# Performance work log

Measured on AMD Instinct MI355X. Metric: run time of the kernel, lower is better.

Reference implementation:

```python
import jax, jax.numpy as jnp
import numpy as np
from jax import lax

DECAY = 0.9
EPS = 1e-12  # F.normalize eps

B, IN_C, H, W_SP = 32, 512, 64, 64
CODE, CLASSES, MEM = 256, 4, 20


def setup_inputs() -> dict:
    key = jax.random.key(0)
    k1, k2, k3, k4, k5 = jax.random.split(key, 5)
    feats = jax.random.normal(k1, (B, IN_C, H, W_SP), dtype=jnp.float32)
    preds = jax.random.uniform(k2, (B, 1, H, W_SP), dtype=jnp.float32)
    labels = jax.random.randint(k3, (B,), 0, CLASSES, dtype=jnp.int64)
    # queue buffer, L2-normalized along code dim as in __init__
    q = jax.random.normal(k4, (CLASSES, MEM, CODE), dtype=jnp.float32)
    queue = q / jnp.maximum(jnp.linalg.norm(q, axis=2, keepdims=True), EPS)
    kw, kb = jax.random.split(k5)
    Wp = jax.random.normal(kw, (CODE, IN_C), dtype=jnp.float32) * (1.0 / np.sqrt(IN_C))
    bp = jax.random.normal(kb, (CODE,), dtype=jnp.float32) * 0.01
    return {"feats": feats, "preds": preds, "labels": labels, "flag": 1,
            "queue": queue, "Wp": Wp, "bp": bp}


def _update_queue(keys, preds, labels, queue):
    # keys: [B, C, H, W] projected feats; preds: [B, 1, H, W]; sequential EMA per sample
    masked = keys * preds                      # broadcast mask
    feat = masked.reshape(keys.shape[0], keys.shape[1], -1).mean(axis=2)  # [B, C]

    def step(q, inp):
        f, l = inp                             # f: [C], l: scalar label
        slot = q[l]                            # [M, C]
        logit = slot @ f                       # [M]  (query @ key)
        upd = logit[:, None] * f[None, :]      # [M, C] (logit @ value.T)
        upd = upd / jnp.maximum(jnp.linalg.norm(upd, axis=1, keepdims=True), EPS)
        q = q.at[l].set(DECAY * slot + (1.0 - DECAY) * upd)
        return q, None

    queue, _ = lax.scan(step, queue, (feat, labels))
    return queue


def reference(feats, preds, labels, flag, queue, Wp, bp):
    # 1x1 conv projection: [B,512,H,W] -> [B,256,H,W]
    x = jnp.einsum('bchw,oc->bohw', feats, Wp) + bp[None, :, None, None]
    if flag == 1:  # 'train' phase: no-grad EMA memory update
        queue = _update_queue(x, preds, labels, queue)
    b, c, h, w = x.shape
    k = x.reshape(b, c, h * w)                 # key = value-key spatial feats [B, C, HW]
    q = queue[labels]                          # per-sample class memory [B, M, C]
    logit = jnp.einsum('bmc,bcn->bmn', q, k)   # [B, M, HW]
    attn = jax.nn.softmax(logit, axis=1)       # softmax over memory slots (dim=0 per sample)
    new_feat = jnp.einsum('bmc,bmn->bcn', q, attn).reshape(b, c, h, w)
    return jnp.concatenate([new_feat, x], axis=1)  # [B, 2C, H, W]
```

## Files before the change

kernel.cpp:

```cpp
#include <hip/hip_runtime.h>

typedef __attribute__((ext_vector_type(4))) float floatx4;
typedef __attribute__((ext_vector_type(8))) short bf16x8;
typedef __attribute__((ext_vector_type(2))) unsigned int uintx2;
typedef __attribute__((ext_vector_type(4))) unsigned int uintx4;

#define HW   4096
#define CIN  512
#define CODE 256
#define MEM  20
#define NCLS 4
#define NB   32

__device__ __forceinline__ unsigned bf16rn(float f) {
    unsigned u = __float_as_uint(f);
    return u + 0x7fffu + ((u >> 16) & 1u);
}

__device__ __forceinline__ int swz(int row, int slot) {
    return slot ^ ((row >> 2) & 3);
}

__global__ __launch_bounds__(256, 2) void gemm_proj_bf16x3(
    const float* __restrict__ feats,
    const float* __restrict__ Wp,
    const float* __restrict__ bp,
    float* __restrict__ out)
{
    __shared__ unsigned short lds[2][4][128][32];

    const int b   = blockIdx.z;
    const int n0  = blockIdx.x * 128;
    const int o0  = blockIdx.y * 128;
    const int tid = threadIdx.x;
    const int lane = tid & 63;
    const int wid  = tid >> 6;
    const int wm = (wid >> 1) * 64;
    const int wn = (wid & 1) * 64;
    const int lr = lane & 15;
    const int lg = lane >> 4;

    const int ar = tid >> 3;
    const int ac = tid & 7;
    const int bn = tid & 127;
    const int bk = (tid >> 7) * 16;

    const float* fb = feats + (size_t)b * CIN * HW + n0 + bn;
    const float* wa = Wp + (size_t)(o0 + ar) * CIN + ac * 4;

    floatx4 acc[4][4];
#pragma unroll
    for (int i = 0; i < 4; ++i)
#pragma unroll
        for (int j = 0; j < 4; ++j)
#pragma unroll
            for (int r = 0; r < 4; ++r) acc[i][j][r] = 0.f;

    floatx4 av[4];
    float   bv[16];

#define G_LOAD(K0)                                                            \
    {                                                                         \
        _Pragma("unroll")                                                     \
        for (int i = 0; i < 4; ++i)                                           \
            av[i] = *(const floatx4*)(wa + (size_t)(32 * i) * CIN + (K0));    \
        _Pragma("unroll")                                                     \
        for (int j = 0; j < 16; ++j)                                          \
            bv[j] = fb[(size_t)((K0) + bk + j) * HW];                         \
    }

#define STAGE(BUF)                                                            \
    {                                                                         \
        _Pragma("unroll")                                                     \
        for (int i = 0; i < 4; ++i) {                                         \
            const int m = ar + 32 * i;                                        \
            unsigned h[4], l[4];                                              \
            _Pragma("unroll")                                                 \
            for (int e = 0; e < 4; ++e) {                                     \
                unsigned r = bf16rn(av[i][e]);                                \
                float hf = __uint_as_float(r & 0xffff0000u);                  \
                h[e] = r;                                                     \
                l[e] = bf16rn(av[i][e] - hf);                                 \
            }                                                                 \
            uintx2 tH, tL;                                                    \
            tH[0] = (h[0] >> 16) | (h[1] & 0xffff0000u);                      \
            tH[1] = (h[2] >> 16) | (h[3] & 0xffff0000u);                      \
            tL[0] = (l[0] >> 16) | (l[1] & 0xffff0000u);                      \
            tL[1] = (l[2] >> 16) | (l[3] & 0xffff0000u);                      \
            const int sA = swz(m, ac >> 1) * 8 + (ac & 1) * 4;                \
            *(uintx2*)&lds[BUF][0][m][sA] = tH;                               \
            *(uintx2*)&lds[BUF][1][m][sA] = tL;                               \
        }                                                                     \
        unsigned ph[8], pl[8];                                                \
        _Pragma("unroll")                                                     \
        for (int p = 0; p < 8; ++p) {                                         \
            unsigned r0 = bf16rn(bv[2 * p]), r1 = bf16rn(bv[2 * p + 1]);      \
            float h0 = __uint_as_float(r0 & 0xffff0000u);                     \
            float h1 = __uint_as_float(r1 & 0xffff0000u);                     \
            unsigned q0 = bf16rn(bv[2 * p] - h0);                             \
            unsigned q1 = bf16rn(bv[2 * p + 1] - h1);                         \
            ph[p] = (r0 >> 16) | (r1 & 0xffff0000u);                          \
            pl[p] = (q0 >> 16) | (q1 & 0xffff0000u);                          \
        }                                                                     \
        const int sb2 = (tid >> 7) * 2;                                       \
        _Pragma("unroll")                                                     \
        for (int u = 0; u < 2; ++u) {                                         \
            const int s = swz(bn, sb2 + u) * 8;                               \
            uintx4 tB, tC;                                                    \
            tB[0] = ph[4 * u];     tB[1] = ph[4 * u + 1];                     \
            tB[2] = ph[4 * u + 2]; tB[3] = ph[4 * u + 3];                     \
            tC[0] = pl[4 * u];     tC[1] = pl[4 * u + 1];                     \
            tC[2] = pl[4 * u + 2]; tC[3] = pl[4 * u + 3];                     \
            *(uintx4*)&lds[BUF][2][bn][s] = tB;                               \
            *(uintx4*)&lds[BUF][3][bn][s] = tC;                               \
        }                                                                     \
    }

#define COMPUTE(BUF)                                                          \
    {                                                                         \
        bf16x8 fah[4], fal[4], fbh[4], fbl[4];                                \
        _Pragma("unroll")                                                     \
        for (int i = 0; i < 4; ++i) {                                         \
            const int rm = wm + i * 16 + lr;                                  \
            const int rn = wn + i * 16 + lr;                                  \
            fah[i] = *(const bf16x8*)&lds[BUF][0][rm][swz(rm, lg) * 8];       \
            fal[i] = *(const bf16x8*)&lds[BUF][1][rm][swz(rm, lg) * 8];       \
            fbh[i] = *(const bf16x8*)&lds[BUF][2][rn][swz(rn, lg) * 8];       \
            fbl[i] = *(const bf16x8*)&lds[BUF][3][rn][swz(rn, lg) * 8];       \
        }                                                                     \
        _Pragma("unroll")                                                     \
        for (int i = 0; i < 4; ++i)                                           \
            _Pragma("unroll")                                                 \
            for (int j = 0; j < 4; ++j) {                                     \
                acc[i][j] = __builtin_amdgcn_mfma_f32_16x16x32_bf16(          \
                    fah[i], fbh[j], acc[i][j], 0, 0, 0);                      \
                acc[i][j] = __builtin_amdgcn_mfma_f32_16x16x32_bf16(          \
                    fah[i], fbl[j], acc[i][j], 0, 0, 0);                      \
                acc[i][j] = __builtin_amdgcn_mfma_f32_16x16x32_bf16(          \
                    fal[i], fbh[j], acc[i][j], 0, 0, 0);                      \
            }                                                                 \
    }

    G_LOAD(0);
    STAGE(0);

#pragma unroll 2
    for (int step = 0; step < 16; ++step) {
        const int cb = step & 1;
        __syncthreads();
        if (step < 15) G_LOAD((step + 1) * 32);
        COMPUTE(cb);
        if (step < 15) STAGE(cb ^ 1);
    }

#undef G_LOAD
#undef STAGE
#undef COMPUTE

#pragma unroll
    for (int i = 0; i < 4; ++i) {
#pragma unroll
        for (int r = 0; r < 4; ++r) {
            const int m = o0 + wm + i * 16 + lg * 4 + r;
            const float bias = bp[m];
            float* orow = out + ((size_t)b * 2 * CODE + CODE + m) * HW
                        + n0 + wn + lr;
#pragma unroll
            for (int j = 0; j < 4; ++j)
                orow[j * 16] = acc[i][j][r] + bias;
        }
    }
}

__global__ __launch_bounds__(256) void featmean_kernel(
    const float* __restrict__ preds,
    const float* __restrict__ out,
    float* __restrict__ featbuf)
{
    const int c0 = blockIdx.x * 16;
    const int b  = blockIdx.y;
    const int tid = threadIdx.x;
    const int w = tid >> 6, lane = tid & 63;

    __shared__ float sp[HW];
    const float* prow = preds + (size_t)b * HW;
#pragma unroll
    for (int j = 0; j < 4; ++j)
        *(floatx4*)&sp[tid * 4 + j * 1024] = *(const floatx4*)(prow + tid * 4 + j * 1024);
    __syncthreads();

    for (int cc = 0; cc < 4; ++cc) {
        const int c = c0 + w * 4 + cc;
        const float* xrow = out + ((size_t)b * 2 * CODE + CODE + c) * HW;
        float s = 0.f;
#pragma unroll 4
        for (int j = 0; j < 16; ++j) {
            floatx4 xv = *(const floatx4*)(xrow + lane * 4 + j * 256);
            floatx4 pv = *(const floatx4*)&sp[lane * 4 + j * 256];
            s += xv[0] * pv[0] + xv[1] * pv[1] + xv[2] * pv[2] + xv[3] * pv[3];
        }
        for (int off = 32; off > 0; off >>= 1) s += __shfl_down(s, off, 64);
        if (lane == 0) featbuf[b * CODE + c] = s * (1.f / HW);
    }
}

__global__ __launch_bounds__(256) void scan_kernel(
    const float* __restrict__ queue_in,
    const float* __restrict__ featbuf,
    const int* __restrict__ labels,
    const int* __restrict__ flag,
    float* __restrict__ qbuf)
{
    const int tid = threadIdx.x;
    for (int i = tid; i < NCLS * MEM * CODE; i += 256)
        qbuf[i] = queue_in[i];
    __syncthreads();
    if (*flag != 1) return;

    __shared__ float sf[CODE];
    __shared__ float sred[256];
    __shared__ float slog[MEM];
    __shared__ float scoef[MEM];
    __shared__ float snorm;

    const int w = tid >> 6, lane = tid & 63;

    for (int b = 0; b < NB; ++b) {
        const int l = labels[b] & 3;
        float f = featbuf[b * CODE + tid];
        sf[tid] = f;
        sred[tid] = f * f;
        __syncthreads();
        for (int st = 128; st > 0; st >>= 1) {
            if (tid < st) sred[tid] += sred[tid + st];
            __syncthreads();
        }
        if (tid == 0) snorm = sqrtf(sred[0]);
        __syncthreads();

        float* qrow = qbuf + (size_t)l * MEM * CODE;
        for (int mm = 0; mm < 5; ++mm) {
            int m = w * 5 + mm;
            float p = 0.f;
#pragma unroll
            for (int j = 0; j < 4; ++j) {
                int c = lane + 64 * j;
                p += qrow[m * CODE + c] * sf[c];
            }
            for (int off = 32; off > 0; off >>= 1) p += __shfl_down(p, off, 64);
            if (lane == 0) slog[m] = p;
        }
        __syncthreads();
        if (tid < MEM) {
            float lg = slog[tid];
            float denom = fmaxf(fabsf(lg) * snorm, 1e-12f);
            scoef[tid] = 0.1f * lg / denom;
        }
        __syncthreads();
        for (int m = 0; m < MEM; ++m) {
            int idx = m * CODE + tid;
            qrow[idx] = 0.9f * qrow[idx] + scoef[m] * sf[tid];
        }
        __syncthreads();
    }
}

__global__ __launch_bounds__(256) void attn_kernel(
    const float* __restrict__ qbuf,
    const int* __restrict__ labels,
    float* __restrict__ out)
{
    const int b = blockIdx.y;
    const int n = blockIdx.x * 256 + threadIdx.x;
    const int l = labels[b] & 3;

    __shared__ float sq[MEM * CODE];
    for (int i = threadIdx.x; i < MEM * CODE; i += 256)
        sq[i] = qbuf[(size_t)l * MEM * CODE + i];
    __syncthreads();

    const float* xb = out + ((size_t)b * 2 * CODE + CODE) * HW;

    float lg[MEM];
#pragma unroll
    for (int m = 0; m < MEM; ++m) lg[m] = 0.f;

    for (int c = 0; c < CODE; ++c) {
        float xv = xb[(size_t)c * HW + n];
#pragma unroll
        for (int m = 0; m < MEM; ++m) lg[m] += sq[m * CODE + c] * xv;
    }

    float mx = lg[0];
#pragma unroll
    for (int m = 1; m < MEM; ++m) mx = fmaxf(mx, lg[m]);
    float s = 0.f;
#pragma unroll
    for (int m = 0; m < MEM; ++m) { lg[m] = __expf(lg[m] - mx); s += lg[m]; }
    const float inv = 1.f / s;

    float* ob = out + (size_t)b * 2 * CODE * HW;
    for (int c = 0; c < CODE; ++c) {
        float acc = 0.f;
#pragma unroll
        for (int m = 0; m < MEM; ++m) acc += sq[m * CODE + c] * lg[m];
        ob[(size_t)c * HW + n] = acc * inv;
    }
}

extern "C" void kernel_launch(void* const* d_in, const int* in_sizes, int n_in,
                              void* d_out, int out_size, void* d_ws, size_t ws_size,
                              hipStream_t stream)
{
    const float* feats  = (const float*)d_in[0];
    const float* preds  = (const float*)d_in[1];
    const int*   labels = (const int*)d_in[2];
    const int*   flag   = (const int*)d_in[3];
    const float* queue  = (const float*)d_in[4];
    const float* Wp     = (const float*)d_in[5];
    const float* bp     = (const float*)d_in[6];
    float* out = (float*)d_out;

    float* featbuf = (float*)d_ws;
    float* qbuf    = featbuf + NB * CODE;

    gemm_proj_bf16x3<<<dim3(HW / 128, CODE / 128, NB), 256, 0, stream>>>(feats, Wp, bp, out);
    featmean_kernel<<<dim3(16, NB), 256, 0, stream>>>(preds, out, featbuf);
    scan_kernel<<<1, 256, 0, stream>>>(queue, featbuf, labels, flag, qbuf);
    attn_kernel<<<dim3(HW / 256, NB), 256, 0, stream>>>(qbuf, labels, out);
}
```

Baseline: 665.8 us.

## Move attention to bf16x3 MFMA and keep per-class scan in registers

The scalar per-pixel attention kernel becomes an MFMA kernel. It splits the queue and the activations into bf16 hi/lo pairs to approximate fp32 logits, computes the softmax from the accumulator fragments, and runs the value matmul with the bf16-rounded probabilities. The EMA scan kernel assigns one wavefront per class and keeps that class's queue in registers, removing the block-wide syncs and shared-memory reductions. The risk is precision: the probabilities are rounded to bf16 and only the hi/lo split of the queue is kept in the second matmul.

Result: faster. 597.7 us (-10.2%).

```diff
diff --git a/kernel.cpp b/kernel.cpp
--- a/kernel.cpp
+++ b/kernel.cpp
@@ -211,100 +211,172 @@
     const int* __restrict__ flag,
     float* __restrict__ qbuf)
 {
-    const int tid = threadIdx.x;
-    for (int i = tid; i < NCLS * MEM * CODE; i += 256)
-        qbuf[i] = queue_in[i];
-    __syncthreads();
-    if (*flag != 1) return;
-
-    __shared__ float sf[CODE];
-    __shared__ float sred[256];
-    __shared__ float slog[MEM];
-    __shared__ float scoef[MEM];
-    __shared__ float snorm;
-
-    const int w = tid >> 6, lane = tid & 63;
-
-    for (int b = 0; b < NB; ++b) {
-        const int l = labels[b] & 3;
-        float f = featbuf[b * CODE + tid];
-        sf[tid] = f;
-        sred[tid] = f * f;
-        __syncthreads();
-        for (int st = 128; st > 0; st >>= 1) {
-            if (tid < st) sred[tid] += sred[tid + st];
-            __syncthreads();
-        }
-        if (tid == 0) snorm = sqrtf(sred[0]);
-        __syncthreads();
-
-        float* qrow = qbuf + (size_t)l * MEM * CODE;
-        for (int mm = 0; mm < 5; ++mm) {
-            int m = w * 5 + mm;
-            float p = 0.f;
-#pragma unroll
-            for (int j = 0; j < 4; ++j) {
-                int c = lane + 64 * j;
-                p += qrow[m * CODE + c] * sf[c];
+    const int tid  = threadIdx.x;
+    const int w    = tid >> 6;
+    const int lane = tid & 63;
+
+    float qreg[MEM][4];
+    const float* qr = queue_in + (size_t)w * MEM * CODE;
+#pragma unroll
+    for (int m = 0; m < MEM; ++m)
+#pragma unroll
+        for (int j = 0; j < 4; ++j)
+            qreg[m][j] = qr[m * CODE + lane + 64 * j];
+
+    if (*flag == 1) {
+        for (int b = 0; b < NB; ++b) {
+            const int l = labels[b] & 3;
+            if (l != w) continue;
+            float f[4];
+#pragma unroll
+            for (int j = 0; j < 4; ++j) f[j] = featbuf[b * CODE + lane + 64 * j];
+            float n2 = f[0] * f[0] + f[1] * f[1] + f[2] * f[2] + f[3] * f[3];
+#pragma unroll
+            for (int off = 1; off < 64; off <<= 1) n2 += __shfl_xor(n2, off, 64);
+            const float nrm = sqrtf(n2);
+#pragma unroll
+            for (int m = 0; m < MEM; ++m) {
+                float p = qreg[m][0] * f[0] + qreg[m][1] * f[1]
+                        + qreg[m][2] * f[2] + qreg[m][3] * f[3];
+#pragma unroll
+                for (int off = 1; off < 64; off <<= 1) p += __shfl_xor(p, off, 64);
+                const float coef = 0.1f * p / fmaxf(fabsf(p) * nrm, 1e-12f);
+#pragma unroll
+                for (int j = 0; j < 4; ++j)
+                    qreg[m][j] = 0.9f * qreg[m][j] + coef * f[j];
             }
-            for (int off = 32; off > 0; off >>= 1) p += __shfl_down(p, off, 64);
-            if (lane == 0) slog[m] = p;
-        }
-        __syncthreads();
-        if (tid < MEM) {
-            float lg = slog[tid];
-            float denom = fmaxf(fabsf(lg) * snorm, 1e-12f);
-            scoef[tid] = 0.1f * lg / denom;
-        }
-        __syncthreads();
-        for (int m = 0; m < MEM; ++m) {
-            int idx = m * CODE + tid;
-            qrow[idx] = 0.9f * qrow[idx] + scoef[m] * sf[tid];
-        }
-        __syncthreads();
-    }
-}
-
-__global__ __launch_bounds__(256) void attn_kernel(
+        }
+    }
+
+    float* qo = qbuf + (size_t)w * MEM * CODE;
+#pragma unroll
+    for (int m = 0; m < MEM; ++m)
+#pragma unroll
+        for (int j = 0; j < 4; ++j)
+            qo[m * CODE + lane + 64 * j] = qreg[m][j];
+}
+
+__global__ __launch_bounds__(256, 2) void attn_mfma(
     const float* __restrict__ qbuf,
     const int* __restrict__ labels,
     float* __restrict__ out)
 {
-    const int b = blockIdx.y;
-    const int n = blockIdx.x * 256 + threadIdx.x;
-    const int l = labels[b] & 3;
-
-    __shared__ float sq[MEM * CODE];
-    for (int i = threadIdx.x; i < MEM * CODE; i += 256)
-        sq[i] = qbuf[(size_t)l * MEM * CODE + i];
+    __shared__ unsigned short sqh[32][256];
+    __shared__ unsigned short sql[32][256];
+    __shared__ unsigned short qth[256][40];
+    __shared__ unsigned short qtl[256][40];
+    __shared__ unsigned short pb[4][16][32];
+
+    const int b    = blockIdx.y;
+    const int n0   = blockIdx.x * 256;
+    const int tid  = threadIdx.x;
+    const int lane = tid & 63;
+    const int wid  = tid >> 6;
+    const int lidx = lane & 15;
+    const int g    = lane >> 4;
+    const int l    = labels[b] & 3;
+
+    const float* qsrc = qbuf + (size_t)l * MEM * CODE;
+    for (int idx = tid; idx < 32 * 256; idx += 256) {
+        const int m = idx >> 8, c = idx & 255;
+        const float v = (m < MEM) ? qsrc[m * CODE + c] : 0.f;
+        const unsigned rh = bf16rn(v);
+        const float hf = __uint_as_float(rh & 0xffff0000u);
+        const unsigned rl = bf16rn(v - hf);
+        const unsigned short h16 = (unsigned short)(rh >> 16);
+        const unsigned short l16 = (unsigned short)(rl >> 16);
+        const int cs = (((c >> 3) ^ (m & 7)) << 3) | (c & 7);
+        sqh[m][cs] = h16;
+        sql[m][cs] = l16;
+        qth[c][m] = h16;
+        qtl[c][m] = l16;
+    }
     __syncthreads();
 
     const float* xb = out + ((size_t)b * 2 * CODE + CODE) * HW;
-
-    float lg[MEM];
-#pragma unroll
-    for (int m = 0; m < MEM; ++m) lg[m] = 0.f;
-
-    for (int c = 0; c < CODE; ++c) {
-        float xv = xb[(size_t)c * HW + n];
-#pragma unroll
-        for (int m = 0; m < MEM; ++m) lg[m] += sq[m * CODE + c] * xv;
-    }
-
-    float mx = lg[0];
-#pragma unroll
-    for (int m = 1; m < MEM; ++m) mx = fmaxf(mx, lg[m]);
-    float s = 0.f;
-#pragma unroll
-    for (int m = 0; m < MEM; ++m) { lg[m] = __expf(lg[m] - mx); s += lg[m]; }
-    const float inv = 1.f / s;
-
     float* ob = out + (size_t)b * 2 * CODE * HW;
-    for (int c = 0; c < CODE; ++c) {
-        float acc = 0.f;
-#pragma unroll
-        for (int m = 0; m < MEM; ++m) acc += sq[m * CODE + c] * lg[m];
-        ob[(size_t)c * HW + n] = acc * inv;
+
+    for (int ns = 0; ns < 4; ++ns) {
+        const int nb = n0 + wid * 64 + ns * 16;
+        const float* xcol = xb + nb + lidx;
+
+        float xr[64];
+#pragma unroll
+        for (int ks = 0; ks < 8; ++ks)
+#pragma unroll
+            for (int j = 0; j < 8; ++j)
+                xr[ks * 8 + j] = xcol[(size_t)(ks * 32 + g * 8 + j) * HW];
+
+        floatx4 acc0 = {0.f, 0.f, 0.f, 0.f};
+        floatx4 acc1 = {0.f, 0.f, 0.f, 0.f};
+
+#pragma unroll
+        for (int ks = 0; ks < 8; ++ks) {
+            union { uintx4 u; bf16x8 v; } cvh, cvl;
+#pragma unroll
+            for (int p = 0; p < 4; ++p) {
+                const float a0 = xr[ks * 8 + 2 * p];
+                const float a1 = xr[ks * 8 + 2 * p + 1];
+                const unsigned r0 = bf16rn(a0), r1 = bf16rn(a1);
+                const float h0 = __uint_as_float(r0 & 0xffff0000u);
+                const float h1 = __uint_as_float(r1 & 0xffff0000u);
+                const unsigned q0 = bf16rn(a0 - h0), q1 = bf16rn(a1 - h1);
+                cvh.u[p] = (r0 >> 16) | (r1 & 0xffff0000u);
+                cvl.u[p] = (q0 >> 16) | (q1 & 0xffff0000u);
+            }
+            const int s2 = ((ks * 4 + g) ^ (lidx & 7)) * 8;
+            const bf16x8 a0h = *(const bf16x8*)&sqh[lidx][s2];
+            const bf16x8 a0l = *(const bf16x8*)&sql[lidx][s2];
+            const bf16x8 a1h = *(const bf16x8*)&sqh[16 + lidx][s2];
+            const bf16x8 a1l = *(const bf16x8*)&sql[16 + lidx][s2];
+            acc0 = __builtin_amdgcn_mfma_f32_16x16x32_bf16(a0h, cvh.v, acc0, 0, 0, 0);
+            acc0 = __builtin_amdgcn_mfma_f32_16x16x32_bf16(a0h, cvl.v, acc0, 0, 0, 0);
+            acc0 = __builtin_amdgcn_mfma_f32_16x16x32_bf16(a0l, cvh.v, acc0, 0, 0, 0);
+            acc1 = __builtin_amdgcn_mfma_f32_16x16x32_bf16(a1h, cvh.v, acc1, 0, 0, 0);
+            acc1 = __builtin_amdgcn_mfma_f32_16x16x32_bf16(a1h, cvl.v, acc1, 0, 0, 0);
+            acc1 = __builtin_amdgcn_mfma_f32_16x16x32_bf16(a1l, cvh.v, acc1, 0, 0, 0);
+        }
+
+        float mx = fmaxf(fmaxf(acc0[0], acc0[1]), fmaxf(acc0[2], acc0[3]));
+        if (g == 0)
+            mx = fmaxf(mx, fmaxf(fmaxf(acc1[0], acc1[1]), fmaxf(acc1[2], acc1[3])));
+        mx = fmaxf(mx, __shfl_xor(mx, 16, 64));
+        mx = fmaxf(mx, __shfl_xor(mx, 32, 64));
+
+        float e0[4], e1[4], s = 0.f;
+#pragma unroll
+        for (int r = 0; r < 4; ++r) { e0[r] = __expf(acc0[r] - mx); s += e0[r]; }
+#pragma unroll
+        for (int r = 0; r < 4; ++r) {
+            e1[r] = (g == 0) ? __expf(acc1[r] - mx) : 0.f;
+            s += e1[r];
+        }
+        s += __shfl_xor(s, 16, 64);
+        s += __shfl_xor(s, 32, 64);
+        const float inv = 1.f / s;
+
+        const unsigned pw0 = (bf16rn(e0[0] * inv) >> 16) | (bf16rn(e0[1] * inv) & 0xffff0000u);
+        const unsigned pw1 = (bf16rn(e0[2] * inv) >> 16) | (bf16rn(e0[3] * inv) & 0xffff0000u);
+        const unsigned pw2 = (bf16rn(e1[0] * inv) >> 16) | (bf16rn(e1[1] * inv) & 0xffff0000u);
+        const unsigned pw3 = (bf16rn(e1[2] * inv) >> 16) | (bf16rn(e1[3] * inv) & 0xffff0000u);
+        *(unsigned*)&pb[wid][lidx][g * 4]          = pw0;
+        *(unsigned*)&pb[wid][lidx][g * 4 + 2]      = pw1;
+        *(unsigned*)&pb[wid][lidx][16 + g * 4]     = pw2;
+        *(unsigned*)&pb[wid][lidx][16 + g * 4 + 2] = pw3;
+
+        const bf16x8 pfrag = *(const bf16x8*)&pb[wid][lidx][g * 8];
+
+#pragma unroll
+        for (int ct = 0; ct < 16; ++ct) {
+            const bf16x8 ath = *(const bf16x8*)&qth[ct * 16 + lidx][g * 8];
+            const bf16x8 atl = *(const bf16x8*)&qtl[ct * 16 + lidx][g * 8];
+            floatx4 f4 = {0.f, 0.f, 0.f, 0.f};
+            f4 = __builtin_amdgcn_mfma_f32_16x16x32_bf16(ath, pfrag, f4, 0, 0, 0);
+            f4 = __builtin_amdgcn_mfma_f32_16x16x32_bf16(atl, pfrag, f4, 0, 0, 0);
+            float* orow = ob + (size_t)(ct * 16 + g * 4) * HW + nb + lidx;
+#pragma unroll
+            for (int r = 0; r < 4; ++r) orow[(size_t)r * HW] = f4[r];
+        }
     }
 }
 
@@ -327,5 +399,5 @@
     gemm_proj_bf16x3<<<dim3(HW / 128, CODE / 128, NB), 256, 0, stream>>>(feats, Wp, bp, out);
     featmean_kernel<<<dim3(16, NB), 256, 0, stream>>>(preds, out, featbuf);
     scan_kernel<<<1, 256, 0, stream>>>(queue, featbuf, labels, flag, qbuf);
-    attn_kernel<<<dim3(HW / 256, NB), 256, 0, stream>>>(qbuf, labels, out);
-}
+    attn_mfma<<<dim3(HW / 256, NB), 256, 0, stream>>>(qbuf, labels, out);
+}
```
